# Performance work log

Measured on AMD Instinct MI355X. Metric: run time of the kernel, lower is better.

## Reference

```python
import jax, jax.numpy as jnp
import numpy as np

N_NODES = 100000
N_EDGES = 1600000
IN_F, HID_F, OUT_F = 128, 128, 128


def setup_inputs() -> dict:
    key = jax.random.key(0)
    k1, k2, k3, k4, k5, k6 = jax.random.split(key, 6)
    x = jax.random.normal(k1, (N_NODES, IN_F), dtype=jnp.float32)
    edge_index = jax.random.randint(k2, (2, N_EDGES), 0, N_NODES, dtype=jnp.int32)
    # nn.Linear params (PyTorch layout: W [out, in], y = x @ W.T + b)
    s1 = 1.0 / np.sqrt(IN_F)
    W1 = jax.random.uniform(k3, (HID_F, IN_F), minval=-s1, maxval=s1, dtype=jnp.float32)
    b1 = jax.random.uniform(k4, (HID_F,), minval=-s1, maxval=s1, dtype=jnp.float32)
    s2 = 1.0 / np.sqrt(HID_F)
    W2 = jax.random.uniform(k5, (OUT_F, HID_F), minval=-s2, maxval=s2, dtype=jnp.float32)
    b2 = jax.random.uniform(k6, (OUT_F,), minval=-s2, maxval=s2, dtype=jnp.float32)
    return {"x": x, "edge_index": edge_index, "W1": W1, "b1": b1, "W2": W2, "b2": b2}


def _spmm_mean(h, row, col, deg_inv):
    # (adj @ h)[i] = sum_{edges e: row[e]==i} h[col[e]], then scale by deg_inv[i]
    agg = jax.ops.segment_sum(h[col], row, num_segments=N_NODES)
    return agg * deg_inv[:, None]


def reference(x, edge_index, W1, b1, W2, b2):
    row, col = edge_index[0], edge_index[1]
    # degree = row-sum of adjacency (duplicates in COO are summed, matching torch)
    deg = jax.ops.segment_sum(jnp.ones((N_EDGES,), dtype=x.dtype), row, num_segments=N_NODES)
    deg_inv = jnp.where(deg > 0, 1.0 / deg, 0.0)
    # dropout in eval mode = identity
    h = x @ W1.T + b1
    h = _spmm_mean(h, row, col, deg_inv)
    h = jax.nn.elu(h)
    h = h @ W2.T + b2
    h = _spmm_mean(h, row, col, deg_inv)
    return h
```

## Files before the change

### kernel.cpp

```cpp
#include <hip/hip_runtime.h>
#include <math.h>

#define N_NODES 100000
#define N_EDGES 1600000
#define F 128
#define NBUCK 391
#define EPB 4096
#define CAP 4800

#define XCH512 (N_NODES * F / 8 / 512)
#define WCH512 (F * F / 2 / 512)

typedef _Float16 f16x2 __attribute__((ext_vector_type(2)));
typedef _Float16 f16x8 __attribute__((ext_vector_type(8)));
typedef __fp16 fp16x2 __attribute__((ext_vector_type(2)));
typedef float f32x2 __attribute__((ext_vector_type(2)));
typedef float f32x4 __attribute__((ext_vector_type(4)));

__device__ inline uint pkrtz(float a, float b) {
    union { fp16x2 h; uint u; } c;
    c.h = __builtin_amdgcn_cvt_pkrtz(a, b);
    return c.u;
}
__device__ inline f16x2 as2(uint u) {
    union { uint u; f16x2 h; } c; c.u = u; return c.h;
}

__device__ inline int wave_incl_scan(int v, int lane) {
#pragma unroll
    for (int off = 1; off < 64; off <<= 1) {
        int t = __shfl_up(v, off);
        if (lane >= off) v += t;
    }
    return v;
}


__global__ __launch_bounds__(512) void build_convert_kernel(
        const int* __restrict__ row, const int* __restrict__ col,
        int* __restrict__ bucket_cursor, int* __restrict__ pairs,
        const float* __restrict__ X, const float* __restrict__ W1,
        const float* __restrict__ W2, uint* __restrict__ Xh,
        uint* __restrict__ W1h, uint* __restrict__ W2h) {
    __shared__ int stage[EPB];
    __shared__ ushort bid[EPB];
    __shared__ int lcnt[NBUCK], lcur[NBUCK], loff[NBUCK], gbase[NBUCK];
    __shared__ int wsum[8];
    const int blk = blockIdx.x;
    const int tid = threadIdx.x;

    if (blk >= NBUCK) {
        if (blk < NBUCK + XCH512) {
            int i = (blk - NBUCK) * 512 + tid;
            float4 a = *(const float4*)&X[(size_t)i * 8];
            float4 c = *(const float4*)&X[(size_t)i * 8 + 4];
            uint4 o = {pkrtz(a.x, a.y), pkrtz(a.z, a.w), pkrtz(c.x, c.y), pkrtz(c.z, c.w)};
            *(uint4*)&Xh[(size_t)i * 4] = o;
        } else {
            int i = (blk - NBUCK - XCH512) * 512 + tid;
            float2 a = *(const float2*)&W1[i * 2];
            float2 c = *(const float2*)&W2[i * 2];
            W1h[i] = pkrtz(a.x, a.y);
            W2h[i] = pkrtz(c.x, c.y);
        }
        return;
    }

    const int lane = tid & 63;
    const int wid = tid >> 6;
    const int base = blk * EPB;
    const int cnt = min(N_EDGES - base, EPB);

    for (int i = tid; i < NBUCK; i += 512) { lcnt[i] = 0; lcur[i] = 0; }
    __syncthreads();
    for (int i = 0; i < EPB / 512; ++i) {
        int e = base + i * 512 + tid;
        if (e < N_EDGES) atomicAdd(&lcnt[row[e] >> 8], 1);
    }
    __syncthreads();
    {
        int v = (tid < NBUCK) ? lcnt[tid] : 0;
        int inc = wave_incl_scan(v, lane);
        if (lane == 63) wsum[wid] = inc;
        __syncthreads();
        if (tid == 0) {
            int a = 0;
#pragma unroll
            for (int i = 0; i < 8; ++i) { int t = wsum[i]; wsum[i] = a; a += t; }
        }
        __syncthreads();
        if (tid < NBUCK) loff[tid] = inc - v + wsum[wid];
    }
    if (tid < NBUCK) {
        int c = lcnt[tid];
        gbase[tid] = c ? atomicAdd(&bucket_cursor[tid], c) : 0;
    }
    __syncthreads();
    for (int i = 0; i < EPB / 512; ++i) {
        int e = base + i * 512 + tid;
        if (e < N_EDGES) {
            int r = row[e], c = col[e];
            int b = r >> 8;
            int rk = atomicAdd(&lcur[b], 1);
            int q = loff[b] + rk;
            stage[q] = ((r & 255) << 17) | c;
            bid[q] = (ushort)b;
        }
    }
    __syncthreads();
    for (int q = tid; q < cnt; q += 512) {
        int b = bid[q];
        int t = gbase[b] + (q - loff[b]);
        if (t < CAP) pairs[b * CAP + t] = stage[q];
    }
}

__global__ __launch_bounds__(1024) void csr_finalize_kernel(const int* __restrict__ pairs,
                                                            const int* __restrict__ bucket_cursor,
                                                            int* __restrict__ csr_col,
                                                            int2* __restrict__ rs,
                                                            float* __restrict__ deg_inv) {
    __shared__ int stage2[CAP];
    __shared__ int colstage[CAP];
    __shared__ int rcnt[256], rcnt2[256], roff[256];
    __shared__ int wsum[4];
    const int tid = threadIdx.x;
    const int lane = tid & 63;
    const int wid = tid >> 6;
    const int b = blockIdx.x;
    const int cnt = min(bucket_cursor[b], CAP);
    const int base = b * CAP;

    if (tid < 256) { rcnt[tid] = 0; rcnt2[tid] = 0; }
    for (int q = tid; q < cnt; q += 1024) stage2[q] = pairs[base + q];
    __syncthreads();
    for (int q = tid; q < cnt; q += 1024) atomicAdd(&rcnt[stage2[q] >> 17], 1);
    __syncthreads();
    int d = 0, inc = 0;
    if (tid < 256) {
        d = rcnt[tid];
        inc = wave_incl_scan(d, lane);
        if (lane == 63) wsum[wid] = inc;
    }
    __syncthreads();
    if (tid == 0) {
        int a = 0;
#pragma unroll
        for (int i = 0; i < 4; ++i) { int t = wsum[i]; wsum[i] = a; a += t; }
    }
    __syncthreads();
    if (tid < 256) {
        const int excl = inc - d + wsum[wid];
        roff[tid] = excl;
        const int grow = (b << 8) + tid;
        if (grow < N_NODES) {
            rs[grow] = make_int2(base + excl, d);
            deg_inv[grow] = d ? 1.0f / (float)d : 0.0f;
        }
    }
    __syncthreads();
    for (int q = tid; q < cnt; q += 1024) {
        int v = stage2[q];
        int lr = v >> 17;
        int rk = atomicAdd(&rcnt2[lr], 1);
        colstage[roff[lr] + rk] = v & 0x1FFFF;
    }
    __syncthreads();
    for (int q = tid; q < cnt; q += 1024) csr_col[base + q] = colstage[q];
}


template <bool ELU, bool OUT_F32>
__global__ __launch_bounds__(256, 8) void fused_agg_gemm_kernel(
        const ushort* __restrict__ H,
        const int2* __restrict__ rs,
        const int* __restrict__ csr_col,
        const float* __restrict__ deg_inv,
        const ushort* __restrict__ Wh,
        const float* __restrict__ bias,
        void* __restrict__ out) {
    __shared__ __align__(16) ushort xs[16 * 136];

    const int tid = threadIdx.x;
    const int m0 = blockIdx.x << 4;
    const int g = tid >> 4;
    const int fo = (tid & 15) << 3;

    {
        const int node = m0 + g;
        f32x2 a[4];
#pragma unroll
        for (int i = 0; i < 4; ++i) a[i] = (f32x2){0.f, 0.f};
        const int2 sd = rs[node];
        int p = sd.x;
        const int e = sd.x + sd.y;
        const float di = deg_inv[node];
        if (p + 7 < e) {
            int cc[8];
#pragma unroll
            for (int k = 0; k < 8; ++k) cc[k] = __builtin_nontemporal_load(&csr_col[p + k]);
            while (true) {
                uint4 vv[8];
#pragma unroll
                for (int k = 0; k < 8; ++k) vv[k] = *(const uint4*)&H[(size_t)cc[k] * F + fo];
                p += 8;
                const bool more = (p + 7 < e);
                int cn[8];
                if (more) {
#pragma unroll
                    for (int k = 0; k < 8; ++k) cn[k] = __builtin_nontemporal_load(&csr_col[p + k]);
                }
                asm volatile("" :: "v"(vv[0].x), "v"(vv[1].x), "v"(vv[2].x), "v"(vv[3].x),
                                   "v"(vv[4].x), "v"(vv[5].x), "v"(vv[6].x), "v"(vv[7].x));
#pragma unroll
                for (int k = 0; k < 8; k += 4) {
                    f16x2 h0 = (as2(vv[k].x) + as2(vv[k + 1].x)) + (as2(vv[k + 2].x) + as2(vv[k + 3].x));
                    f16x2 h1 = (as2(vv[k].y) + as2(vv[k + 1].y)) + (as2(vv[k + 2].y) + as2(vv[k + 3].y));
                    f16x2 h2 = (as2(vv[k].z) + as2(vv[k + 1].z)) + (as2(vv[k + 2].z) + as2(vv[k + 3].z));
                    f16x2 h3 = (as2(vv[k].w) + as2(vv[k + 1].w)) + (as2(vv[k + 2].w) + as2(vv[k + 3].w));
                    a[0] += (f32x2){(float)h0.x, (float)h0.y};
                    a[1] += (f32x2){(float)h1.x, (float)h1.y};
                    a[2] += (f32x2){(float)h2.x, (float)h2.y};
                    a[3] += (f32x2){(float)h3.x, (float)h3.y};
                }
                if (!more) break;
#pragma unroll
                for (int k = 0; k < 8; ++k) cc[k] = cn[k];
            }
        }
        if (p + 3 < e) {
            int c0 = csr_col[p], c1 = csr_col[p + 1], c2 = csr_col[p + 2], c3 = csr_col[p + 3];
            uint4 v0 = *(const uint4*)&H[(size_t)c0 * F + fo];
            uint4 v1 = *(const uint4*)&H[(size_t)c1 * F + fo];
            uint4 v2 = *(const uint4*)&H[(size_t)c2 * F + fo];
            uint4 v3 = *(const uint4*)&H[(size_t)c3 * F + fo];
            f16x2 h0 = (as2(v0.x) + as2(v1.x)) + (as2(v2.x) + as2(v3.x));
            f16x2 h1 = (as2(v0.y) + as2(v1.y)) + (as2(v2.y) + as2(v3.y));
            f16x2 h2 = (as2(v0.z) + as2(v1.z)) + (as2(v2.z) + as2(v3.z));
            f16x2 h3 = (as2(v0.w) + as2(v1.w)) + (as2(v2.w) + as2(v3.w));
            a[0] += (f32x2){(float)h0.x, (float)h0.y};
            a[1] += (f32x2){(float)h1.x, (float)h1.y};
            a[2] += (f32x2){(float)h2.x, (float)h2.y};
            a[3] += (f32x2){(float)h3.x, (float)h3.y};
            p += 4;
        }
        if (p + 1 < e) {
            int c0 = csr_col[p], c1 = csr_col[p + 1];
            uint4 v0 = *(const uint4*)&H[(size_t)c0 * F + fo];
            uint4 v1 = *(const uint4*)&H[(size_t)c1 * F + fo];
            f16x2 h0 = as2(v0.x) + as2(v1.x);
            f16x2 h1 = as2(v0.y) + as2(v1.y);
            f16x2 h2 = as2(v0.z) + as2(v1.z);
            f16x2 h3 = as2(v0.w) + as2(v1.w);
            a[0] += (f32x2){(float)h0.x, (float)h0.y};
            a[1] += (f32x2){(float)h1.x, (float)h1.y};
            a[2] += (f32x2){(float)h2.x, (float)h2.y};
            a[3] += (f32x2){(float)h3.x, (float)h3.y};
            p += 2;
        }
        if (p < e) {
            int c = csr_col[p];
            uint4 v = *(const uint4*)&H[(size_t)c * F + fo];
            f16x2 h0 = as2(v.x), h1 = as2(v.y), h2 = as2(v.z), h3 = as2(v.w);
            a[0] += (f32x2){(float)h0.x, (float)h0.y};
            a[1] += (f32x2){(float)h1.x, (float)h1.y};
            a[2] += (f32x2){(float)h2.x, (float)h2.y};
            a[3] += (f32x2){(float)h3.x, (float)h3.y};
        }
        uint4 o = {pkrtz(a[0].x * di, a[0].y * di), pkrtz(a[1].x * di, a[1].y * di),
                   pkrtz(a[2].x * di, a[2].y * di), pkrtz(a[3].x * di, a[3].y * di)};
        *(uint4*)&xs[g * 136 + fo] = o;
    }
    __syncthreads();

    const int w = tid >> 6;
    const int lane = tid & 63;
    const int q = lane >> 4;
    const int t = lane & 15;

    f16x8 xfr[4];
#pragma unroll
    for (int kk = 0; kk < 4; ++kk)
        xfr[kk] = *(const f16x8*)&xs[t * 136 + kk * 32 + q * 8];

    if (!OUT_F32) __syncthreads();

    const int node = m0 + t;
    const float dv = deg_inv[node];
    const float mk = (dv > 0.f) ? 1.f : 0.f;

    f32x4 vout[2];
#pragma unroll
    for (int jj = 0; jj < 2; ++jj) {
        const int j = (w << 1) | jj;
        f32x4 acc = (f32x4){0.f, 0.f, 0.f, 0.f};
        const ushort* wrow = &Wh[(j * 16 + t) * F + q * 8];
#pragma unroll
        for (int kk = 0; kk < 4; ++kk) {
            f16x8 wfr = *(const f16x8*)&wrow[kk * 32];
            acc = __builtin_amdgcn_mfma_f32_16x16x32_f16(wfr, xfr[kk], acc, 0, 0, 0);
        }
        f32x4 bb = *(const f32x4*)&bias[j * 16 + q * 4];
        f32x4 v = acc + bb * mk;
        if (ELU) {
#pragma unroll
            for (int r = 0; r < 4; ++r) v[r] = (v[r] > 0.f) ? v[r] : expm1f(v[r]);
        }
        vout[jj] = v;
    }

    if (OUT_F32) {
        float* of = &((float*)out)[(size_t)node * F + (w << 5) + q * 4];
        __builtin_nontemporal_store(vout[0], (f32x4*)of);
        __builtin_nontemporal_store(vout[1], (f32x4*)(of + 16));
    } else {
        ushort* ys = xs;
        uint2 o0 = {pkrtz(vout[0][0], vout[0][1]), pkrtz(vout[0][2], vout[0][3])};
        uint2 o1 = {pkrtz(vout[1][0], vout[1][1]), pkrtz(vout[1][2], vout[1][3])};
        *(uint2*)&ys[t * 136 + (w << 5) + q * 4] = o0;
        *(uint2*)&ys[t * 136 + (w << 5) + 16 + q * 4] = o1;
        __syncthreads();
        const int n2 = tid >> 4, seg = tid & 15;
        uint4 vo = *(const uint4*)&ys[n2 * 136 + seg * 8];
        __builtin_nontemporal_store(*(f32x4*)&vo,
            (f32x4*)&((ushort*)out)[(size_t)(m0 + n2) * F + seg * 8]);
    }
}


extern "C" void kernel_launch(void* const* d_in, const int* in_sizes, int n_in,
                              void* d_out, int out_size, void* d_ws, size_t ws_size,
                              hipStream_t stream) {
    const float* x  = (const float*)d_in[0];
    const int*   ei = (const int*)d_in[1];
    const float* W1 = (const float*)d_in[2];
    const float* b1 = (const float*)d_in[3];
    const float* W2 = (const float*)d_in[4];
    const float* b2 = (const float*)d_in[5];
    float* out = (float*)d_out;

    const int* row = ei;
    const int* col = ei + N_EDGES;

    ushort* bufA = (ushort*)d_ws;
    ushort* bufB = bufA + (size_t)N_NODES * F;
    int* csr_col = (int*)(bufB + (size_t)N_NODES * F);
    int2* rs = (int2*)(csr_col + NBUCK * CAP);
    float* deg_inv = (float*)(rs + N_NODES + 4);
    int* bucket_cursor = (int*)(deg_inv + N_NODES);
    uint* W1h = (uint*)(bucket_cursor + 512);
    uint* W2h = W1h + F * F / 2;
    int* pairs = (int*)bufA;

    (void)hipMemsetAsync(bucket_cursor, 0, 512 * sizeof(int), stream);
    build_convert_kernel<<<NBUCK + XCH512 + WCH512, 512, 0, stream>>>(
        row, col, bucket_cursor, pairs, x, W1, W2, (uint*)bufB, W1h, W2h);
    csr_finalize_kernel<<<NBUCK, 1024, 0, stream>>>(pairs, bucket_cursor, csr_col, rs, deg_inv);

    const int fb = N_NODES / 16;
    fused_agg_gemm_kernel<true, false><<<fb, 256, 0, stream>>>(
        (const ushort*)bufB, rs, csr_col, deg_inv, (const ushort*)W1h, b1, bufA);
    fused_agg_gemm_kernel<false, true><<<fb, 256, 0, stream>>>(
        bufA, rs, csr_col, deg_inv, (const ushort*)W2h, b2, out);
}
```

Baseline: 271.1 us.

## Split each node's neighbor list across two thread halves and stage edges in LDS

The fused aggregate+GEMM kernel now runs 512 threads per 16-node block. Each node's neighbor range is split in half between two thread groups, whose fp32 partial sums are reduced in shared memory before the fp16 conversion. Each wave then computes one 16-column MFMA tile instead of two, and the fp32 output is staged through LDS for coalesced stores. The bucket-build kernel loads row/col once into shared memory instead of reading row twice from global memory. The cost is more LDS per block, which may reduce occupancy, plus extra barriers.

Result: slower. 362.5 us (+33.7%).

```diff
diff --git a/kernel.cpp b/kernel.cpp
--- a/kernel.cpp
+++ b/kernel.cpp
@@ -42,7 +42,7 @@
         const float* __restrict__ X, const float* __restrict__ W1,
         const float* __restrict__ W2, uint* __restrict__ Xh,
         uint* __restrict__ W1h, uint* __restrict__ W2h) {
-    __shared__ int stage[EPB];
+    __shared__ int rowst[EPB], colst[EPB], stage[EPB];
     __shared__ ushort bid[EPB];
     __shared__ int lcnt[NBUCK], lcur[NBUCK], loff[NBUCK], gbase[NBUCK];
     __shared__ int wsum[8];
@@ -72,11 +72,14 @@
     const int cnt = min(N_EDGES - base, EPB);
 
     for (int i = tid; i < NBUCK; i += 512) { lcnt[i] = 0; lcur[i] = 0; }
-    __syncthreads();
+#pragma unroll
     for (int i = 0; i < EPB / 512; ++i) {
-        int e = base + i * 512 + tid;
-        if (e < N_EDGES) atomicAdd(&lcnt[row[e] >> 8], 1);
-    }
+        int idx = i * 512 + tid;
+        int e = base + idx;
+        if (e < N_EDGES) { rowst[idx] = row[e]; colst[idx] = col[e]; }
+    }
+    __syncthreads();
+    for (int idx = tid; idx < cnt; idx += 512) atomicAdd(&lcnt[rowst[idx] >> 8], 1);
     __syncthreads();
     {
         int v = (tid < NBUCK) ? lcnt[tid] : 0;
@@ -96,16 +99,13 @@
         gbase[tid] = c ? atomicAdd(&bucket_cursor[tid], c) : 0;
     }
     __syncthreads();
-    for (int i = 0; i < EPB / 512; ++i) {
-        int e = base + i * 512 + tid;
-        if (e < N_EDGES) {
-            int r = row[e], c = col[e];
-            int b = r >> 8;
-            int rk = atomicAdd(&lcur[b], 1);
-            int q = loff[b] + rk;
-            stage[q] = ((r & 255) << 17) | c;
-            bid[q] = (ushort)b;
-        }
+    for (int idx = tid; idx < cnt; idx += 512) {
+        int r = rowst[idx], c = colst[idx];
+        int b = r >> 8;
+        int rk = atomicAdd(&lcur[b], 1);
+        int q = loff[b] + rk;
+        stage[q] = ((r & 255) << 17) | c;
+        bid[q] = (ushort)b;
     }
     __syncthreads();
     for (int q = tid; q < cnt; q += 512) {
@@ -171,7 +171,7 @@
 
 
 template <bool ELU, bool OUT_F32>
-__global__ __launch_bounds__(256, 8) void fused_agg_gemm_kernel(
+__global__ __launch_bounds__(512, 8) void fused_agg_gemm_kernel(
         const ushort* __restrict__ H,
         const int2* __restrict__ rs,
         const int* __restrict__ csr_col,
@@ -179,22 +179,24 @@
         const ushort* __restrict__ Wh,
         const float* __restrict__ bias,
         void* __restrict__ out) {
-    __shared__ __align__(16) ushort xs[16 * 136];
+    __shared__ __align__(16) float xsf[2][16][132];
 
     const int tid = threadIdx.x;
     const int m0 = blockIdx.x << 4;
-    const int g = tid >> 4;
+    const int gg = tid >> 4;
+    const int n = gg & 15;
+    const int h = gg >> 4;
     const int fo = (tid & 15) << 3;
 
     {
-        const int node = m0 + g;
+        const int node = m0 + n;
         f32x2 a[4];
 #pragma unroll
         for (int i = 0; i < 4; ++i) a[i] = (f32x2){0.f, 0.f};
         const int2 sd = rs[node];
-        int p = sd.x;
-        const int e = sd.x + sd.y;
-        const float di = deg_inv[node];
+        const int d2 = sd.y >> 1;
+        int p = sd.x + (h ? d2 : 0);
+        const int e = h ? (sd.x + sd.y) : (sd.x + d2);
         if (p + 7 < e) {
             int cc[8];
 #pragma unroll
@@ -267,9 +269,9 @@
             a[2] += (f32x2){(float)h2.x, (float)h2.y};
             a[3] += (f32x2){(float)h3.x, (float)h3.y};
         }
-        uint4 o = {pkrtz(a[0].x * di, a[0].y * di), pkrtz(a[1].x * di, a[1].y * di),
-                   pkrtz(a[2].x * di, a[2].y * di), pkrtz(a[3].x * di, a[3].y * di)};
-        *(uint4*)&xs[g * 136 + fo] = o;
+        float* dst = &xsf[h][n][fo];
+        *(f32x4*)dst = (f32x4){a[0].x, a[0].y, a[1].x, a[1].y};
+        *(f32x4*)(dst + 4) = (f32x4){a[2].x, a[2].y, a[3].x, a[3].y};
     }
     __syncthreads();
 
@@ -277,53 +279,55 @@
     const int lane = tid & 63;
     const int q = lane >> 4;
     const int t = lane & 15;
+    const float dv = deg_inv[m0 + t];
+    const float mk = (dv > 0.f) ? 1.f : 0.f;
 
     f16x8 xfr[4];
 #pragma unroll
-    for (int kk = 0; kk < 4; ++kk)
-        xfr[kk] = *(const f16x8*)&xs[t * 136 + kk * 32 + q * 8];
-
-    if (!OUT_F32) __syncthreads();
-
-    const int node = m0 + t;
-    const float dv = deg_inv[node];
-    const float mk = (dv > 0.f) ? 1.f : 0.f;
-
-    f32x4 vout[2];
-#pragma unroll
-    for (int jj = 0; jj < 2; ++jj) {
-        const int j = (w << 1) | jj;
-        f32x4 acc = (f32x4){0.f, 0.f, 0.f, 0.f};
-        const ushort* wrow = &Wh[(j * 16 + t) * F + q * 8];
-#pragma unroll
-        for (int kk = 0; kk < 4; ++kk) {
-            f16x8 wfr = *(const f16x8*)&wrow[kk * 32];
-            acc = __builtin_amdgcn_mfma_f32_16x16x32_f16(wfr, xfr[kk], acc, 0, 0, 0);
-        }
-        f32x4 bb = *(const f32x4*)&bias[j * 16 + q * 4];
-        f32x4 v = acc + bb * mk;
-        if (ELU) {
-#pragma unroll
-            for (int r = 0; r < 4; ++r) v[r] = (v[r] > 0.f) ? v[r] : expm1f(v[r]);
-        }
-        vout[jj] = v;
+    for (int kk = 0; kk < 4; ++kk) {
+        const float* p0 = &xsf[0][t][kk * 32 + q * 8];
+        const float* p1 = &xsf[1][t][kk * 32 + q * 8];
+        f32x4 u0 = *(const f32x4*)p0, u1 = *(const f32x4*)(p0 + 4);
+        f32x4 v0 = *(const f32x4*)p1, v1 = *(const f32x4*)(p1 + 4);
+        f32x4 s0 = (u0 + v0) * dv, s1 = (u1 + v1) * dv;
+        union { uint4 u; f16x8 hh; } cv;
+        cv.u = (uint4){pkrtz(s0.x, s0.y), pkrtz(s0.z, s0.w), pkrtz(s1.x, s1.y), pkrtz(s1.z, s1.w)};
+        xfr[kk] = cv.hh;
+    }
+    __syncthreads();
+
+    f32x4 acc = (f32x4){0.f, 0.f, 0.f, 0.f};
+    const ushort* wrow = &Wh[(w * 16 + t) * F + q * 8];
+#pragma unroll
+    for (int kk = 0; kk < 4; ++kk) {
+        f16x8 wfr = *(const f16x8*)&wrow[kk * 32];
+        acc = __builtin_amdgcn_mfma_f32_16x16x32_f16(wfr, xfr[kk], acc, 0, 0, 0);
+    }
+    f32x4 bb = *(const f32x4*)&bias[w * 16 + q * 4];
+    f32x4 v = acc + bb * mk;
+    if (ELU) {
+#pragma unroll
+        for (int r = 0; r < 4; ++r) v[r] = (v[r] > 0.f) ? v[r] : expm1f(v[r]);
     }
 
     if (OUT_F32) {
-        float* of = &((float*)out)[(size_t)node * F + (w << 5) + q * 4];
-        __builtin_nontemporal_store(vout[0], (f32x4*)of);
-        __builtin_nontemporal_store(vout[1], (f32x4*)(of + 16));
+        float* ysf = (float*)xsf;
+        *(f32x4*)&ysf[t * 132 + (w << 4) + q * 4] = v;
+        __syncthreads();
+        const int n3 = tid >> 5, seg = tid & 31;
+        f32x4 vo = *(const f32x4*)&ysf[n3 * 132 + seg * 4];
+        __builtin_nontemporal_store(vo, (f32x4*)&((float*)out)[(size_t)(m0 + n3) * F + seg * 4]);
     } else {
-        ushort* ys = xs;
-        uint2 o0 = {pkrtz(vout[0][0], vout[0][1]), pkrtz(vout[0][2], vout[0][3])};
-        uint2 o1 = {pkrtz(vout[1][0], vout[1][1]), pkrtz(vout[1][2], vout[1][3])};
-        *(uint2*)&ys[t * 136 + (w << 5) + q * 4] = o0;
-        *(uint2*)&ys[t * 136 + (w << 5) + 16 + q * 4] = o1;
+        ushort* ys16 = (ushort*)xsf;
+        uint2 o0 = {pkrtz(v[0], v[1]), pkrtz(v[2], v[3])};
+        *(uint2*)&ys16[t * 136 + (w << 4) + q * 4] = o0;
         __syncthreads();
-        const int n2 = tid >> 4, seg = tid & 15;
-        uint4 vo = *(const uint4*)&ys[n2 * 136 + seg * 8];
-        __builtin_nontemporal_store(*(f32x4*)&vo,
-            (f32x4*)&((ushort*)out)[(size_t)(m0 + n2) * F + seg * 8]);
+        if (tid < 256) {
+            const int n2 = tid >> 4, seg = tid & 15;
+            uint4 vo = *(const uint4*)&ys16[n2 * 136 + seg * 8];
+            __builtin_nontemporal_store(*(f32x4*)&vo,
+                (f32x4*)&((ushort*)out)[(size_t)(m0 + n2) * F + seg * 8]);
+        }
     }
 }
 
@@ -358,8 +362,8 @@
     csr_finalize_kernel<<<NBUCK, 1024, 0, stream>>>(pairs, bucket_cursor, csr_col, rs, deg_inv);
 
     const int fb = N_NODES / 16;
-    fused_agg_gemm_kernel<true, false><<<fb, 256, 0, stream>>>(
+    fused_agg_gemm_kernel<true, false><<<fb, 512, 0, stream>>>(
         (const ushort*)bufB, rs, csr_col, deg_inv, (const ushort*)W1h, b1, bufA);
-    fused_agg_gemm_kernel<false, true><<<fb, 256, 0, stream>>>(
+    fused_agg_gemm_kernel<false, true><<<fb, 512, 0, stream>>>(
         bufA, rs, csr_col, deg_inv, (const ushort*)W2h, b2, out);
 }
```

## Make each wave compute its own 4 nodes' GEMM to drop block barriers

Applied to the files above, without the earlier changes.

Each wave now aggregates 4 nodes and runs all 8 output MFMA tiles for those same nodes, with its B operand replicated across lanes. Because a wave only reads and writes its own rows of shared memory, the block-wide __syncthreads calls between aggregation, the GEMM and the output staging are removed. The cost is 4x more MFMA work and weight loads per wave, since only 4 of the 16 MFMA columns hold useful data, plus a separate fp32 staging buffer in shared memory that may reduce occupancy.

Result: slower. 394.3 us (+45.4%).

```diff
diff --git a/kernel.cpp b/kernel.cpp
--- a/kernel.cpp
+++ b/kernel.cpp
@@ -180,14 +180,17 @@
         const float* __restrict__ bias,
         void* __restrict__ out) {
     __shared__ __align__(16) ushort xs[16 * 136];
+    __shared__ __align__(16) char ysraw[16 * 132 * 4];
 
     const int tid = threadIdx.x;
     const int m0 = blockIdx.x << 4;
-    const int g = tid >> 4;
-    const int fo = (tid & 15) << 3;
+    const int wv = tid >> 6;
+    const int lane = tid & 63;
+    const int n = (wv << 2) | (lane >> 4);
+    const int fo = (lane & 15) << 3;
 
     {
-        const int node = m0 + g;
+        const int node = m0 + n;
         f32x2 a[4];
 #pragma unroll
         for (int i = 0; i < 4; ++i) a[i] = (f32x2){0.f, 0.f};
@@ -269,30 +272,26 @@
         }
         uint4 o = {pkrtz(a[0].x * di, a[0].y * di), pkrtz(a[1].x * di, a[1].y * di),
                    pkrtz(a[2].x * di, a[2].y * di), pkrtz(a[3].x * di, a[3].y * di)};
-        *(uint4*)&xs[g * 136 + fo] = o;
-    }
-    __syncthreads();
-
-    const int w = tid >> 6;
-    const int lane = tid & 63;
+        *(uint4*)&xs[n * 136 + fo] = o;
+    }
+
     const int q = lane >> 4;
     const int t = lane & 15;
+    const int tr = (wv << 2) | (t & 3);
 
     f16x8 xfr[4];
 #pragma unroll
     for (int kk = 0; kk < 4; ++kk)
-        xfr[kk] = *(const f16x8*)&xs[t * 136 + kk * 32 + q * 8];
-
-    if (!OUT_F32) __syncthreads();
-
-    const int node = m0 + t;
-    const float dv = deg_inv[node];
+        xfr[kk] = *(const f16x8*)&xs[tr * 136 + kk * 32 + q * 8];
+
+    const float dv = deg_inv[m0 + tr];
     const float mk = (dv > 0.f) ? 1.f : 0.f;
 
-    f32x4 vout[2];
-#pragma unroll
-    for (int jj = 0; jj < 2; ++jj) {
-        const int j = (w << 1) | jj;
+    ushort* ys16 = (ushort*)ysraw;
+    float* ys32 = (float*)ysraw;
+
+#pragma unroll
+    for (int j = 0; j < 8; ++j) {
         f32x4 acc = (f32x4){0.f, 0.f, 0.f, 0.f};
         const ushort* wrow = &Wh[(j * 16 + t) * F + q * 8];
 #pragma unroll
@@ -306,24 +305,28 @@
 #pragma unroll
             for (int r = 0; r < 4; ++r) v[r] = (v[r] > 0.f) ? v[r] : expm1f(v[r]);
         }
-        vout[jj] = v;
-    }
-
+        if (t < 4) {
+            const int rrow = (wv << 2) + t;
+            if (OUT_F32) {
+                *(f32x4*)&ys32[rrow * 132 + j * 16 + q * 4] = v;
+            } else {
+                uint2 o = {pkrtz(v[0], v[1]), pkrtz(v[2], v[3])};
+                *(uint2*)&ys16[rrow * 136 + j * 16 + q * 4] = o;
+            }
+        }
+    }
+    const int row = (wv << 2) + (lane >> 4);
+    const int sg = lane & 15;
     if (OUT_F32) {
-        float* of = &((float*)out)[(size_t)node * F + (w << 5) + q * 4];
-        __builtin_nontemporal_store(vout[0], (f32x4*)of);
-        __builtin_nontemporal_store(vout[1], (f32x4*)(of + 16));
+        f32x4 a0 = *(const f32x4*)&ys32[row * 132 + sg * 4];
+        f32x4 a1 = *(const f32x4*)&ys32[row * 132 + (sg + 16) * 4];
+        float* of = &((float*)out)[(size_t)(m0 + row) * F];
+        __builtin_nontemporal_store(a0, (f32x4*)&of[sg * 4]);
+        __builtin_nontemporal_store(a1, (f32x4*)&of[(sg + 16) * 4]);
     } else {
-        ushort* ys = xs;
-        uint2 o0 = {pkrtz(vout[0][0], vout[0][1]), pkrtz(vout[0][2], vout[0][3])};
-        uint2 o1 = {pkrtz(vout[1][0], vout[1][1]), pkrtz(vout[1][2], vout[1][3])};
-        *(uint2*)&ys[t * 136 + (w << 5) + q * 4] = o0;
-        *(uint2*)&ys[t * 136 + (w << 5) + 16 + q * 4] = o1;
-        __syncthreads();
-        const int n2 = tid >> 4, seg = tid & 15;
-        uint4 vo = *(const uint4*)&ys[n2 * 136 + seg * 8];
+        uint4 vo = *(const uint4*)&ys16[row * 136 + sg * 8];
         __builtin_nontemporal_store(*(f32x4*)&vo,
-            (f32x4*)&((ushort*)out)[(size_t)(m0 + n2) * F + seg * 8]);
+            (f32x4*)&((ushort*)out)[(size_t)(m0 + row) * F + sg * 8]);
     }
 }
 
```
